# Kernel optimization log

Measured on AMD Instinct MI355X. Metric: run time of the kernel, lower is better.

## Reference

```python
import jax, jax.numpy as jnp
import numpy as np

N = 4096  # square [B, T+1] as required by original indexing (T = shape[0], indexed on dim 1)
GAMMA = 0.99

def setup_inputs() -> dict:
    key = jax.random.key(0)
    ks = jax.random.split(key, 6)
    shape = (N, N)
    names = ["Q", "expected_target_Q", "target_Q", "rewards",
             "target_policy_probs", "behaviour_policy_probs"]
    return {n: jax.random.normal(k, shape, dtype=jnp.float32) for n, k in zip(names, ks)}

def _retrace_loss(Q, expected_target_Q, target_Q, rewards,
                  target_policy_probs, behaviour_policy_probs):
    rewards = rewards * 100.0
    # retrace weights c_t = exp(min(log pi - log b, 0)) = min(1, pi/b)
    c_ret = jnp.exp(jnp.minimum(target_policy_probs - behaviour_policy_probs, 0.0))
    T = Q.shape[0]  # faithful to original (square inputs => equals time length)
    last = target_Q[:, T - 1]  # Q_ret[:, -1] = target_Q[:, -1]
    # reverse-time linear recurrence via a single scan:
    # Q_ret[t-1] = r[t-1] + gamma*c[t]*(Q_ret[t] - target_Q[t]) + gamma*E[t]
    xs = (rewards[:, :T - 1].T[::-1],          # [T-1, B], t-1 = T-2 .. 0
          c_ret[:, 1:T].T[::-1],               # c[t],  t = T-1 .. 1
          target_Q[:, 1:T].T[::-1],
          expected_target_Q[:, 1:T].T[::-1])

    def step(q_next, x):
        r, c, tq, eq = x
        q = r + GAMMA * c * (q_next - tq) + GAMMA * eq
        return q, q

    _, qs = jax.lax.scan(step, last, xs)       # qs: [T-1, B] for t = T-2 .. 0
    Q_ret = jnp.concatenate([qs[::-1].T, last[:, None]], axis=1)  # [B, T]
    Q_ret = jax.lax.stop_gradient(Q_ret)       # computed under torch.no_grad()
    return jnp.mean((Q - Q_ret) ** 2)

def reference(Q, expected_target_Q, target_Q, rewards,
              target_policy_probs, behaviour_policy_probs):
    return _retrace_loss(Q, expected_target_Q, target_Q, rewards,
                         target_policy_probs, behaviour_policy_probs)
```

## Files before the change

kernel.cpp:

```cpp
#include <hip/hip_runtime.h>


#define NROWS 4096
#define TLEN  4096
#define BLOCK 1024
#define EPT   4
#define NWAVES (BLOCK / 64)

__global__ __launch_bounds__(BLOCK) void retrace_main(
    const float* __restrict__ Q,
    const float* __restrict__ eQ,
    const float* __restrict__ tQ,
    const float* __restrict__ rw,
    const float* __restrict__ tpp,
    const float* __restrict__ bpp,
    double* __restrict__ partials)
{
    constexpr float G = 0.99f;
    __shared__ float sT[NWAVES], sP[NWAVES], sQ[NWAVES], sE[NWAVES];
    __shared__ float sWA[NWAVES], sWB[NWAVES];
    __shared__ float sRed[NWAVES];

    const int tid  = threadIdx.x;
    const int lane = tid & 63;
    const int wv   = tid >> 6;
    const long long base = (long long)blockIdx.x * TLEN;
    const int ua = (TLEN - EPT) - EPT * tid;

    const float4 R4  = *(const float4*)(rw  + base + ua);
    const float4 T4  = *(const float4*)(tpp + base + ua);
    const float4 P4  = *(const float4*)(bpp + base + ua);
    const float4 Tq4 = *(const float4*)(tQ  + base + ua);
    const float4 E4  = *(const float4*)(eQ  + base + ua);
    const float4 Qm4 = *(const float4*)(Q   + base + ua);

    if (lane == 63) { sT[wv] = T4.x; sP[wv] = P4.x; sQ[wv] = Tq4.x; sE[wv] = E4.x; }
    __syncthreads();

    float t4v = __shfl_up(T4.x,  1, 64);
    float p4v = __shfl_up(P4.x,  1, 64);
    float q4v = __shfl_up(Tq4.x, 1, 64);
    float e4v = __shfl_up(E4.x,  1, 64);
    if (lane == 0 && wv > 0) {
        t4v = sT[wv - 1]; p4v = sP[wv - 1]; q4v = sQ[wv - 1]; e4v = sE[wv - 1];
    }

    const float rv[4] = {R4.x,  R4.y,  R4.z,  R4.w};
    const float tv[4] = {T4.x,  T4.y,  T4.z,  T4.w};
    const float pv[4] = {P4.x,  P4.y,  P4.z,  P4.w};
    const float qv[4] = {Tq4.x, Tq4.y, Tq4.z, Tq4.w};
    const float ev[4] = {E4.x,  E4.y,  E4.z,  E4.w};
    const float qm[4] = {Qm4.x, Qm4.y, Qm4.z, Qm4.w};

    float Aa[EPT], Bb[EPT];
    #pragma unroll
    for (int m = 1; m <= EPT - 1; ++m) {
        const float c  = __expf(fminf(tv[m] - pv[m], 0.0f));
        const float gc = G * c;
        Aa[m - 1] = gc;
        Bb[m - 1] = fmaf(100.0f, rv[m - 1], fmaf(-gc, qv[m], G * ev[m]));
    }
    if (tid == 0) {
        Aa[EPT - 1] = 0.0f;
        Bb[EPT - 1] = qv[EPT - 1];
    } else {
        const float c  = __expf(fminf(t4v - p4v, 0.0f));
        const float gc = G * c;
        Aa[EPT - 1] = gc;
        Bb[EPT - 1] = fmaf(100.0f, rv[EPT - 1], fmaf(-gc, q4v, G * e4v));
    }

    float Ac = 1.0f, Bc = 0.0f;
    #pragma unroll
    for (int k = 0; k < EPT; ++k) {
        const int idx = EPT - 1 - k;
        Bc = fmaf(Aa[idx], Bc, Bb[idx]);
        Ac = Aa[idx] * Ac;
    }

    float Ai = Ac, Bi = Bc;
    #pragma unroll
    for (int off = 1; off < 64; off <<= 1) {
        const float Ap = __shfl_up(Ai, off, 64);
        const float Bp = __shfl_up(Bi, off, 64);
        if (lane >= off) {
            Bi = fmaf(Ai, Bp, Bi);
            Ai = Ai * Ap;
        }
    }

    if (lane == 63) { sWA[wv] = Ai; sWB[wv] = Bi; }
    __syncthreads();
    float Bp = 0.0f;
    #pragma unroll
    for (int j = 0; j < NWAVES - 1; ++j)
        if (j < wv) Bp = fmaf(sWA[j], Bp, sWB[j]);

    float Ae = __shfl_up(Ai, 1, 64);
    float Be = __shfl_up(Bi, 1, 64);
    if (lane == 0) { Ae = 1.0f; Be = 0.0f; }
    float y = fmaf(Ae, Bp, Be);

    float acc = 0.0f;
    #pragma unroll
    for (int k = 0; k < EPT; ++k) {
        const int idx = EPT - 1 - k;
        y = fmaf(Aa[idx], y, Bb[idx]);
        const float d = qm[idx] - y;
        acc = fmaf(d, d, acc);
    }

    #pragma unroll
    for (int off = 32; off > 0; off >>= 1)
        acc += __shfl_down(acc, off, 64);
    if (lane == 0) sRed[wv] = acc;
    __syncthreads();
    if (tid == 0) {
        float s = 0.0f;
        #pragma unroll
        for (int j = 0; j < NWAVES; ++j) s += sRed[j];
        partials[blockIdx.x] = (double)s;
    }
}

__global__ __launch_bounds__(256) void retrace_finalize(
    const double* __restrict__ partials, float* __restrict__ out)
{
    __shared__ double sRed[4];
    double s = 0.0;
    for (int i = threadIdx.x; i < NROWS; i += 256) s += partials[i];
    #pragma unroll
    for (int off = 32; off > 0; off >>= 1)
        s += __shfl_down(s, off, 64);
    if ((threadIdx.x & 63) == 0) sRed[threadIdx.x >> 6] = s;
    __syncthreads();
    if (threadIdx.x == 0) {
        const double tot = sRed[0] + sRed[1] + sRed[2] + sRed[3];
        out[0] = (float)(tot / ((double)NROWS * (double)TLEN));
    }
}

extern "C" void kernel_launch(void* const* d_in, const int* in_sizes, int n_in,
                              void* d_out, int out_size, void* d_ws, size_t ws_size,
                              hipStream_t stream)
{
    const float* Q   = (const float*)d_in[0];
    const float* eQ  = (const float*)d_in[1];
    const float* tQ  = (const float*)d_in[2];
    const float* rw  = (const float*)d_in[3];
    const float* tpp = (const float*)d_in[4];
    const float* bpp = (const float*)d_in[5];
    double* partials = (double*)d_ws;

    retrace_main<<<NROWS, BLOCK, 0, stream>>>(Q, eQ, tQ, rw, tpp, bpp, partials);
    retrace_finalize<<<1, 256, 0, stream>>>(partials, (float*)d_out);
}
```

Before: 341.7 us.

## Process each row with one wavefront looping over chunks with register prefetch

Instead of one 1024-thread block per row that uses shared memory and block barriers for the cross-wave scan carry, each wavefront now owns a whole row. It walks the row in 16 chunks of 256 elements, carrying the scan state between chunks in registers, and prefetches the next chunk's loads into registers. This drops all __syncthreads and LDS traffic and lets the grid use 256-thread blocks holding four rows each. In exchange, each wave now runs a serial chain of 16 wave-level scans, so the kernel depends on enough waves being resident to hide memory latency.

Result: no change. 345.7 us (+1.2%).

```diff
diff --git a/kernel.cpp b/kernel.cpp
--- a/kernel.cpp
+++ b/kernel.cpp
@@ -3,9 +3,10 @@
 
 #define NROWS 4096
 #define TLEN  4096
-#define BLOCK 1024
-#define EPT   4
-#define NWAVES (BLOCK / 64)
+#define CHUNK 256
+#define NCHUNK (TLEN / CHUNK)
+#define BLOCK 256
+#define WPB   (BLOCK / 64)
 
 __global__ __launch_bounds__(BLOCK) void retrace_main(
     const float* __restrict__ Q,
@@ -17,110 +18,116 @@
     double* __restrict__ partials)
 {
     constexpr float G = 0.99f;
-    __shared__ float sT[NWAVES], sP[NWAVES], sQ[NWAVES], sE[NWAVES];
-    __shared__ float sWA[NWAVES], sWB[NWAVES];
-    __shared__ float sRed[NWAVES];
+    const int lane = threadIdx.x & 63;
+    const int row  = blockIdx.x * WPB + (threadIdx.x >> 6);
+    const long long base = (long long)row * TLEN;
 
-    const int tid  = threadIdx.x;
-    const int lane = tid & 63;
-    const int wv   = tid >> 6;
-    const long long base = (long long)blockIdx.x * TLEN;
-    const int ua = (TLEN - EPT) - EPT * tid;
+    const int ua0 = (TLEN - 4) - 4 * lane;
 
-    const float4 R4  = *(const float4*)(rw  + base + ua);
-    const float4 T4  = *(const float4*)(tpp + base + ua);
-    const float4 P4  = *(const float4*)(bpp + base + ua);
-    const float4 Tq4 = *(const float4*)(tQ  + base + ua);
-    const float4 E4  = *(const float4*)(eQ  + base + ua);
-    const float4 Qm4 = *(const float4*)(Q   + base + ua);
+    float4 cR  = *(const float4*)(rw  + base + ua0);
+    float4 cT  = *(const float4*)(tpp + base + ua0);
+    float4 cP  = *(const float4*)(bpp + base + ua0);
+    float4 cQt = *(const float4*)(tQ  + base + ua0);
+    float4 cE  = *(const float4*)(eQ  + base + ua0);
+    float4 cQm = *(const float4*)(Q   + base + ua0);
 
-    if (lane == 63) { sT[wv] = T4.x; sP[wv] = P4.x; sQ[wv] = Tq4.x; sE[wv] = E4.x; }
-    __syncthreads();
+    float y_state = 0.0f;
+    float acc     = 0.0f;
+    float pTx = 0.f, pPx = 0.f, pQtx = 0.f, pEx = 0.f;
 
-    float t4v = __shfl_up(T4.x,  1, 64);
-    float p4v = __shfl_up(P4.x,  1, 64);
-    float q4v = __shfl_up(Tq4.x, 1, 64);
-    float e4v = __shfl_up(E4.x,  1, 64);
-    if (lane == 0 && wv > 0) {
-        t4v = sT[wv - 1]; p4v = sP[wv - 1]; q4v = sQ[wv - 1]; e4v = sE[wv - 1];
-    }
+    #pragma unroll 1
+    for (int c = 0; c < NCHUNK; ++c) {
+        float4 nR, nT, nP, nQt, nE, nQm;
+        if (c + 1 < NCHUNK) {
+            const int uan = ua0 - (c + 1) * CHUNK;
+            nR  = *(const float4*)(rw  + base + uan);
+            nT  = *(const float4*)(tpp + base + uan);
+            nP  = *(const float4*)(bpp + base + uan);
+            nQt = *(const float4*)(tQ  + base + uan);
+            nE  = *(const float4*)(eQ  + base + uan);
+            nQm = *(const float4*)(Q   + base + uan);
+        }
 
-    const float rv[4] = {R4.x,  R4.y,  R4.z,  R4.w};
-    const float tv[4] = {T4.x,  T4.y,  T4.z,  T4.w};
-    const float pv[4] = {P4.x,  P4.y,  P4.z,  P4.w};
-    const float qv[4] = {Tq4.x, Tq4.y, Tq4.z, Tq4.w};
-    const float ev[4] = {E4.x,  E4.y,  E4.z,  E4.w};
-    const float qm[4] = {Qm4.x, Qm4.y, Qm4.z, Qm4.w};
+        float t4v = __shfl_up(cT.x,  1, 64);
+        float p4v = __shfl_up(cP.x,  1, 64);
+        float q4v = __shfl_up(cQt.x, 1, 64);
+        float e4v = __shfl_up(cE.x,  1, 64);
+        const float bT = __shfl(pTx,  63, 64);
+        const float bP = __shfl(pPx,  63, 64);
+        const float bQ = __shfl(pQtx, 63, 64);
+        const float bE = __shfl(pEx,  63, 64);
+        if (lane == 0 && c > 0) { t4v = bT; p4v = bP; q4v = bQ; e4v = bE; }
 
-    float Aa[EPT], Bb[EPT];
-    #pragma unroll
-    for (int m = 1; m <= EPT - 1; ++m) {
-        const float c  = __expf(fminf(tv[m] - pv[m], 0.0f));
-        const float gc = G * c;
-        Aa[m - 1] = gc;
-        Bb[m - 1] = fmaf(100.0f, rv[m - 1], fmaf(-gc, qv[m], G * ev[m]));
-    }
-    if (tid == 0) {
-        Aa[EPT - 1] = 0.0f;
-        Bb[EPT - 1] = qv[EPT - 1];
-    } else {
-        const float c  = __expf(fminf(t4v - p4v, 0.0f));
-        const float gc = G * c;
-        Aa[EPT - 1] = gc;
-        Bb[EPT - 1] = fmaf(100.0f, rv[EPT - 1], fmaf(-gc, q4v, G * e4v));
-    }
+        const float rv[4] = {cR.x,  cR.y,  cR.z,  cR.w};
+        const float tv[4] = {cT.x,  cT.y,  cT.z,  cT.w};
+        const float pv[4] = {cP.x,  cP.y,  cP.z,  cP.w};
+        const float qv[4] = {cQt.x, cQt.y, cQt.z, cQt.w};
+        const float ev[4] = {cE.x,  cE.y,  cE.z,  cE.w};
+        const float qm[4] = {cQm.x, cQm.y, cQm.z, cQm.w};
 
-    float Ac = 1.0f, Bc = 0.0f;
-    #pragma unroll
-    for (int k = 0; k < EPT; ++k) {
-        const int idx = EPT - 1 - k;
-        Bc = fmaf(Aa[idx], Bc, Bb[idx]);
-        Ac = Aa[idx] * Ac;
-    }
+        float Aa[4], Bb[4];
+        #pragma unroll
+        for (int m = 1; m <= 3; ++m) {
+            const float cr = __expf(fminf(tv[m] - pv[m], 0.0f));
+            const float gc = G * cr;
+            Aa[m - 1] = gc;
+            Bb[m - 1] = fmaf(100.0f, rv[m - 1], fmaf(-gc, qv[m], G * ev[m]));
+        }
+        if (c == 0 && lane == 0) {
+            Aa[3] = 0.0f;
+            Bb[3] = qv[3];
+        } else {
+            const float cr = __expf(fminf(t4v - p4v, 0.0f));
+            const float gc = G * cr;
+            Aa[3] = gc;
+            Bb[3] = fmaf(100.0f, rv[3], fmaf(-gc, q4v, G * e4v));
+        }
 
-    float Ai = Ac, Bi = Bc;
-    #pragma unroll
-    for (int off = 1; off < 64; off <<= 1) {
-        const float Ap = __shfl_up(Ai, off, 64);
-        const float Bp = __shfl_up(Bi, off, 64);
-        if (lane >= off) {
-            Bi = fmaf(Ai, Bp, Bi);
-            Ai = Ai * Ap;
+        float Ac = 1.0f, Bc = 0.0f;
+        #pragma unroll
+        for (int k = 0; k < 4; ++k) {
+            const int idx = 3 - k;
+            Bc = fmaf(Aa[idx], Bc, Bb[idx]);
+            Ac = Aa[idx] * Ac;
         }
-    }
 
-    if (lane == 63) { sWA[wv] = Ai; sWB[wv] = Bi; }
-    __syncthreads();
-    float Bp = 0.0f;
-    #pragma unroll
-    for (int j = 0; j < NWAVES - 1; ++j)
-        if (j < wv) Bp = fmaf(sWA[j], Bp, sWB[j]);
+        float Ai = Ac, Bi = Bc;
+        #pragma unroll
+        for (int off = 1; off < 64; off <<= 1) {
+            const float Ap = __shfl_up(Ai, off, 64);
+            const float Bp = __shfl_up(Bi, off, 64);
+            if (lane >= off) {
+                Bi = fmaf(Ai, Bp, Bi);
+                Ai = Ai * Ap;
+            }
+        }
 
-    float Ae = __shfl_up(Ai, 1, 64);
-    float Be = __shfl_up(Bi, 1, 64);
-    if (lane == 0) { Ae = 1.0f; Be = 0.0f; }
-    float y = fmaf(Ae, Bp, Be);
+        float Ae = __shfl_up(Ai, 1, 64);
+        float Be = __shfl_up(Bi, 1, 64);
+        if (lane == 0) { Ae = 1.0f; Be = 0.0f; }
+        float y = fmaf(Ae, y_state, Be);
 
-    float acc = 0.0f;
-    #pragma unroll
-    for (int k = 0; k < EPT; ++k) {
-        const int idx = EPT - 1 - k;
-        y = fmaf(Aa[idx], y, Bb[idx]);
-        const float d = qm[idx] - y;
-        acc = fmaf(d, d, acc);
+        #pragma unroll
+        for (int k = 0; k < 4; ++k) {
+            const int idx = 3 - k;
+            y = fmaf(Aa[idx], y, Bb[idx]);
+            const float d = qm[idx] - y;
+            acc = fmaf(d, d, acc);
+        }
+
+        const float A63 = __shfl(Ai, 63, 64);
+        const float B63 = __shfl(Bi, 63, 64);
+        y_state = fmaf(A63, y_state, B63);
+
+        pTx = cT.x; pPx = cP.x; pQtx = cQt.x; pEx = cE.x;
+        cR = nR; cT = nT; cP = nP; cQt = nQt; cE = nE; cQm = nQm;
     }
 
     #pragma unroll
     for (int off = 32; off > 0; off >>= 1)
         acc += __shfl_down(acc, off, 64);
-    if (lane == 0) sRed[wv] = acc;
-    __syncthreads();
-    if (tid == 0) {
-        float s = 0.0f;
-        #pragma unroll
-        for (int j = 0; j < NWAVES; ++j) s += sRed[j];
-        partials[blockIdx.x] = (double)s;
-    }
+    if (lane == 0)
+        partials[row] = (double)acc;
 }
 
 __global__ __launch_bounds__(256) void retrace_finalize(
@@ -152,6 +159,6 @@
     const float* bpp = (const float*)d_in[5];
     double* partials = (double*)d_ws;
 
-    retrace_main<<<NROWS, BLOCK, 0, stream>>>(Q, eQ, tQ, rw, tpp, bpp, partials);
+    retrace_main<<<NROWS / WPB, BLOCK, 0, stream>>>(Q, eQ, tQ, rw, tpp, bpp, partials);
     retrace_finalize<<<1, 256, 0, stream>>>(partials, (float*)d_out);
 }
```
